# Kernel tuning notes

Hardware: AMD Instinct MI355X
Metric: run time of the kernel (lower is better)

The kernel has to match this reference:

```python
import jax, jax.numpy as jnp
import numpy as np

B = 2
L = 1024
D_MODEL = 1024
D_INNER = 2048   # expand * d_model
D_STATE = 16
DT_RANK = 64     # ceil(d_model / 16)
D_CONV = 4


def setup_inputs() -> dict:
    key = jax.random.key(0)
    ks = jax.random.split(key, 8)
    def nrm(k, shape, scale):
        return jax.random.normal(k, shape, dtype=jnp.float32) * scale
    A_log = jnp.log(jnp.tile(jnp.arange(1, D_STATE + 1, dtype=jnp.float32)[None, :], (D_INNER, 1)))
    return dict(
        hidden_states=jax.random.normal(ks[0], (B, L, D_MODEL), dtype=jnp.float32),
        Win=nrm(ks[1], (D_MODEL, 2 * D_INNER), D_MODEL ** -0.5),
        Wx=nrm(ks[2], (D_INNER, DT_RANK + 2 * D_STATE), D_INNER ** -0.5),
        Wdt=nrm(ks[3], (DT_RANK, D_INNER), DT_RANK ** -0.5),
        dt_bias=nrm(ks[4], (D_INNER,), 1.0),
        Wout=nrm(ks[5], (D_INNER, D_MODEL), D_INNER ** -0.5),
        dw_kernel=nrm(ks[6], (D_CONV, D_INNER), 0.2),
        dw_bias=jnp.zeros((D_INNER,), dtype=jnp.float32),
        A_log=A_log,
        Dskip=jnp.ones((D_INNER,), dtype=jnp.float32),
    )


def _causal_depthwise_conv(x, kernel, bias):
    # x: (B, L, D_INNER), kernel: (k, D_INNER); dilation 1, causal left pad
    k = kernel.shape[0]
    Lq = x.shape[1]
    xpad = jnp.pad(x, ((0, 0), (k - 1, 0), (0, 0)))
    y = sum(xpad[:, i:i + Lq, :] * kernel[i] for i in range(k)) + bias
    return jax.nn.silu(y)


def _selective_scan(u, delta, A, Bm, Cm, Dskip, z):
    # u, delta, z: (B, L, D); A: (D, N); Bm, Cm: (B, L, N)
    deltaA = jnp.exp(jnp.einsum('bld,dn->bldn', delta, A))      # (B,L,D,N)
    deltaBu = jnp.einsum('bld,bln,bld->bldn', delta, Bm, u)     # (B,L,D,N)

    def step(x_prev, elems):
        dA, dBu, c = elems                                      # (B,D,N),(B,D,N),(B,N)
        x_new = dA * x_prev + dBu
        y = jnp.einsum('bdn,bn->bd', x_new, c)
        return x_new, y

    x0 = jnp.zeros((u.shape[0], u.shape[2], A.shape[1]), dtype=jnp.float32)
    _, ys = jax.lax.scan(
        step, x0,
        (deltaA.transpose(1, 0, 2, 3), deltaBu.transpose(1, 0, 2, 3), Cm.transpose(1, 0, 2)))
    y = ys.transpose(1, 0, 2) + u * Dskip                        # skip connection
    return y * jax.nn.silu(z)


def reference(hidden_states, Win, Wx, Wdt, dt_bias, Wout, dw_kernel, dw_bias, A_log, Dskip):
    xz = hidden_states @ Win                                     # (B,L,2*D_INNER)
    x, z = jnp.split(xz, 2, axis=-1)
    A = -jnp.exp(A_log)                                          # (D_INNER, D_STATE)
    x = _causal_depthwise_conv(x, dw_kernel, dw_bias)
    x_dbl = x @ Wx                                               # (B,L,DT_RANK+2*N)
    dt, Bm, Cm = jnp.split(x_dbl, [DT_RANK, DT_RANK + D_STATE], axis=-1)
    delta = jax.nn.softplus(dt @ Wdt + dt_bias)                  # delta_bias + softplus
    y = _selective_scan(x, delta, A, Bm, Cm, Dskip, z)
    return y @ Wout
```

## Files before the change

### kernel.cpp

```cpp
#include <hip/hip_runtime.h>
#include <hip/hip_bf16.h>
#include <math.h>

#define B_SZ 2
#define L_SZ 1024
#define DM 1024
#define DI 2048
#define NS 16
#define DTR 64
#define NCHUNK 16
#define CLEN 64
#define XDLD 128
#define KSPLIT 8

typedef unsigned short ushortT;
typedef __attribute__((ext_vector_type(8))) short short8;
typedef __attribute__((ext_vector_type(4))) float floatx4;

__device__ __forceinline__ ushortT f2bf(float f) {
  unsigned u = __float_as_uint(f);
  unsigned r = (u + 0x7fff + ((u >> 16) & 1)) >> 16;
  return (ushortT)r;
}

__device__ __forceinline__ float bf2f(ushortT v) {
  return __uint_as_float((unsigned)v << 16);
}

__device__ __forceinline__ void gl2lds16(const void* g, void* l) {
  __builtin_amdgcn_global_load_lds(
      (const __attribute__((address_space(1))) unsigned int*)g,
      (__attribute__((address_space(3))) unsigned int*)l, 16, 0, 0);
}

__device__ __forceinline__ unsigned stash_addr(unsigned i) {
  return (i >> 10) * 4096 + 1024 + (i & 1023);
}

__device__ __forceinline__ void tr_body(const float* __restrict__ src,
                                        ushortT* __restrict__ dst, int R, int C,
                                        int bx, int by, int tx, int ty,
                                        float (*t)[33]) {
#pragma unroll
  for (int j = 0; j < 4; ++j)
    t[ty + j * 8][tx] = src[(size_t)(by + ty + j * 8) * C + bx + tx];
  __syncthreads();
#pragma unroll
  for (int j = 0; j < 4; ++j)
    dst[(size_t)(bx + ty + j * 8) * R + by + tx] = f2bf(t[tx][ty + j * 8]);
}

__global__ __launch_bounds__(256) void prep_all(
    const float* __restrict__ hidden, ushortT* __restrict__ hidb,
    const float* __restrict__ Win, ushortT* __restrict__ WinT,
    const float* __restrict__ Wx, ushortT* __restrict__ WxT,
    const float* __restrict__ Wdt, ushortT* __restrict__ WdtT,
    const float* __restrict__ Wout, ushortT* __restrict__ WoutT) {
  __shared__ float t[32][33];
  const int blk = blockIdx.x;
  const int tid = threadIdx.x;
  const int tx = tid & 31, ty = tid >> 5;
  if (blk < 2048) {
    const int i = blk * 256 + tid;
    float4 v = ((const float4*)hidden)[i];
    unsigned lo = (unsigned)f2bf(v.x) | ((unsigned)f2bf(v.y) << 16);
    unsigned hi = (unsigned)f2bf(v.z) | ((unsigned)f2bf(v.w) << 16);
    ((uint2*)hidb)[i] = make_uint2(lo, hi);
  } else if (blk < 6144) {
    const int rel = blk - 2048;
    tr_body(Win, WinT, DM, 2 * DI, (rel & 127) * 32, (rel >> 7) * 32, tx, ty, t);
  } else if (blk < 7168) {
    const int rel = blk - 6144;
    const int k = (rel & 7) * 256 + tid;
    const int n = rel >> 3;
    WxT[(size_t)n * DI + k] = (n < 96) ? f2bf(Wx[(size_t)k * 96 + n]) : (ushortT)0;
  } else if (blk < 7296) {
    const int rel = blk - 7168;
    tr_body(Wdt, WdtT, DTR, DI, (rel & 63) * 32, (rel >> 6) * 32, tx, ty, t);
  } else {
    const int rel = blk - 7296;
    tr_body(Wout, WoutT, DI, DM, (rel & 31) * 32, (rel >> 5) * 32, tx, ty, t);
  }
}

__global__ __launch_bounds__(512) void gemm1_big(
    const ushortT* __restrict__ A, int lda,
    const ushortT* __restrict__ BT, int ldb,
    float* __restrict__ C, int ldc, int K) {
  __shared__ __align__(16) char smem[128 * 128 + 128 * 128];
  char* As = smem;
  char* Bs = smem + 128 * 128;
  const int tid = threadIdx.x;
  const int lane = tid & 63;
  const int quad = lane >> 4;
  const int l16 = lane & 15;
  const int wid = tid >> 6;
  const int wm = wid & 1;
  const int wn = wid >> 1;
  const int m0 = blockIdx.y * 128;
  const int n0 = blockIdx.x * 128;

  floatx4 acc[4][2] = {};

  for (int k0 = 0; k0 < K; k0 += 64) {
    for (int i = tid; i < 128 * 8; i += 512) {
      const int r = i >> 3, c = i & 7;
      const int cg = c ^ (r & 7);
      gl2lds16(A + (size_t)(m0 + r) * lda + k0 + cg * 8, As + (i - lane) * 16);
    }
    for (int i = tid; i < 128 * 8; i += 512) {
      const int r = i >> 3, c = i & 7;
      const int cg = c ^ (r & 7);
      gl2lds16(BT + (size_t)(n0 + r) * ldb + k0 + cg * 8, Bs + (i - lane) * 16);
    }
    __syncthreads();

    short8 afr[4][2], bfr[2][2];
#pragma unroll
    for (int i = 0; i < 4; ++i) {
      const int r = wm * 64 + i * 16 + l16;
#pragma unroll
      for (int s = 0; s < 2; ++s)
        afr[i][s] = *(const short8*)(As + r * 128 + (((s * 4 + quad) ^ (r & 7)) * 16));
    }
#pragma unroll
    for (int j = 0; j < 2; ++j) {
      const int r = wn * 32 + j * 16 + l16;
#pragma unroll
      for (int s = 0; s < 2; ++s)
        bfr[j][s] = *(const short8*)(Bs + r * 128 + (((s * 4 + quad) ^ (r & 7)) * 16));
    }
#pragma unroll
    for (int s = 0; s < 2; ++s)
#pragma unroll
      for (int i = 0; i < 4; ++i)
#pragma unroll
        for (int j = 0; j < 2; ++j)
          acc[i][j] = __builtin_amdgcn_mfma_f32_16x16x32_bf16(afr[i][s], bfr[j][s],
                                                              acc[i][j], 0, 0, 0);
    __syncthreads();
  }
#pragma unroll
  for (int i = 0; i < 4; ++i)
#pragma unroll
    for (int j = 0; j < 2; ++j)
#pragma unroll
      for (int r = 0; r < 4; ++r) {
        const int m = m0 + wm * 64 + i * 16 + quad * 4 + r;
        const int n = n0 + wn * 32 + j * 16 + l16;
        C[(size_t)m * ldc + n] = acc[i][j][r];
      }
}

__global__ __launch_bounds__(256) void gemm_out(
    const ushortT* __restrict__ A, int lda,
    const ushortT* __restrict__ BT, int ldb,
    float* __restrict__ C) {
  __shared__ __align__(16) char smem[64 * 128 + 64 * 128];
  char* As = smem;
  char* Bs = smem + 64 * 128;
  const int tid = threadIdx.x;
  const int lane = tid & 63;
  const int quad = lane >> 4;
  const int l16 = lane & 15;
  const int wid = tid >> 6;
  const int wm = wid & 1;
  const int wn = wid >> 1;
  const int m0 = blockIdx.y * 64;
  const int n0 = blockIdx.x * 64;

  floatx4 acc[2][2] = {};

  for (int k0 = 0; k0 < DI; k0 += 64) {
    for (int i = tid; i < 64 * 8; i += 256) {
      const int r = i >> 3, c = i & 7;
      const int cg = c ^ (r & 7);
      gl2lds16(A + (size_t)(m0 + r) * lda + k0 + cg * 8, As + (i - lane) * 16);
    }
    for (int i = tid; i < 64 * 8; i += 256) {
      const int r = i >> 3, c = i & 7;
      const int cg = c ^ (r & 7);
      gl2lds16(BT + (size_t)(n0 + r) * ldb + k0 + cg * 8, Bs + (i - lane) * 16);
    }
    __syncthreads();

    short8 afr[2][2], bfr[2][2];
#pragma unroll
    for (int i = 0; i < 2; ++i) {
      const int m = wm * 32 + i * 16 + l16;
#pragma unroll
      for (int s = 0; s < 2; ++s)
        afr[i][s] = *(const short8*)(As + m * 128 + (((s * 4 + quad) ^ (m & 7)) * 16));
    }
#pragma unroll
    for (int j = 0; j < 2; ++j) {
      const int n = wn * 32 + j * 16 + l16;
#pragma unroll
      for (int s = 0; s < 2; ++s)
        bfr[j][s] = *(const short8*)(Bs + n * 128 + (((s * 4 + quad) ^ (n & 7)) * 16));
    }
#pragma unroll
    for (int s = 0; s < 2; ++s)
#pragma unroll
      for (int i = 0; i < 2; ++i)
#pragma unroll
        for (int j = 0; j < 2; ++j)
          acc[i][j] = __builtin_amdgcn_mfma_f32_16x16x32_bf16(afr[i][s], bfr[j][s],
                                                              acc[i][j], 0, 0, 0);
    __syncthreads();
  }
#pragma unroll
  for (int i = 0; i < 2; ++i)
#pragma unroll
    for (int j = 0; j < 2; ++j)
#pragma unroll
      for (int r = 0; r < 4; ++r) {
        const int m = m0 + wm * 32 + i * 16 + quad * 4 + r;
        const int n = n0 + wn * 32 + j * 16 + l16;
        C[(size_t)m * DM + n] = acc[i][j][r];
      }
}

__global__ __launch_bounds__(256) void gemm_xdbl_mfma(
    const ushortT* __restrict__ xcb, const ushortT* __restrict__ WxT,
    float* __restrict__ part) {
  __shared__ __align__(16) char smem[64 * 64 + 128 * 64];
  char* As = smem;
  char* Bs = smem + 64 * 64;
  const int tid = threadIdx.x;
  const int lane = tid & 63;
  const int quad = lane >> 4;
  const int l16 = lane & 15;
  const int wid = tid >> 6;
  const int wm = wid & 1;
  const int wn = wid >> 1;
  const int m0 = blockIdx.x * 64;
  const int kbase = blockIdx.y * (DI / KSPLIT);

  floatx4 acc[2][4] = {};

  for (int kk = 0; kk < DI / KSPLIT; kk += 32) {
    const int k0 = kbase + kk;
    for (int i = tid; i < 64 * 4; i += 256) {
      const int r = i >> 2, c = i & 3;
      const int cg = c ^ (r & 3);
      gl2lds16(xcb + (size_t)(m0 + r) * DI + k0 + cg * 8, As + (i - lane) * 16);
    }
    for (int i = tid; i < 128 * 4; i += 256) {
      const int r = i >> 2, c = i & 3;
      const int cg = c ^ (r & 3);
      gl2lds16(WxT + (size_t)r * DI + k0 + cg * 8, Bs + (i - lane) * 16);
    }
    __syncthreads();

    short8 afr[2], bfr[4];
#pragma unroll
    for (int i = 0; i < 2; ++i) {
      const int m = wm * 32 + i * 16 + l16;
      afr[i] = *(const short8*)(As + m * 64 + ((quad ^ (m & 3)) * 16));
    }
#pragma unroll
    for (int j = 0; j < 4; ++j) {
      const int n = wn * 64 + j * 16 + l16;
      bfr[j] = *(const short8*)(Bs + n * 64 + ((quad ^ (n & 3)) * 16));
    }
#pragma unroll
    for (int i = 0; i < 2; ++i)
#pragma unroll
      for (int j = 0; j < 4; ++j)
        acc[i][j] = __builtin_amdgcn_mfma_f32_16x16x32_bf16(afr[i], bfr[j],
                                                            acc[i][j], 0, 0, 0);
    __syncthreads();
  }
  float* out = part + (size_t)blockIdx.y * (B_SZ * L_SZ * XDLD);
#pragma unroll
  for (int i = 0; i < 2; ++i)
#pragma unroll
    for (int j = 0; j < 4; ++j)
#pragma unroll
      for (int r = 0; r < 4; ++r) {
        const int m = m0 + wm * 32 + i * 16 + quad * 4 + r;
        const int n = wn * 64 + j * 16 + l16;
        out[(size_t)m * XDLD + n] = acc[i][j][r];
      }
}

__global__ __launch_bounds__(256) void xdbl_reduce(const float* __restrict__ part,
                                                   float* __restrict__ xdbl,
                                                   ushortT* __restrict__ dtb) {
  const int i = blockIdx.x * 256 + threadIdx.x;
  float4 a = ((const float4*)part)[i];
#pragma unroll
  for (int s = 1; s < KSPLIT; ++s) {
    const float4 b = ((const float4*)part)[(size_t)s * (B_SZ * L_SZ * XDLD / 4) + i];
    a.x += b.x; a.y += b.y; a.z += b.z; a.w += b.w;
  }
  ((float4*)xdbl)[i] = a;
  const int row = i >> 5;
  const int c4 = (i & 31) * 4;
  if (c4 < DTR) {
    const unsigned lo = (unsigned)f2bf(a.x) | ((unsigned)f2bf(a.y) << 16);
    const unsigned hi = (unsigned)f2bf(a.z) | ((unsigned)f2bf(a.w) << 16);
    ((uint2*)dtb)[row * (DTR / 4) + (c4 >> 2)] = make_uint2(lo, hi);
  }
}

__global__ __launch_bounds__(256) void conv_silu(
    const float* __restrict__ xz, const float* __restrict__ kern,
    const float* __restrict__ bias, ushortT* __restrict__ xcb) {
  const int d = blockIdx.y * 256 + threadIdx.x;
  const int b = blockIdx.x >> 7;
  const int l0 = (blockIdx.x & 127) * 8;
  const int row0 = b * L_SZ + l0;
  const float k0v = kern[0 * DI + d], k1v = kern[1 * DI + d];
  const float k2v = kern[2 * DI + d], k3v = kern[3 * DI + d];
  float xv[11];
#pragma unroll
  for (int i = 0; i < 11; ++i) {
    const int l = l0 - 3 + i;
    xv[i] = (l >= 0) ? xz[((size_t)(b * L_SZ + l)) * 4096 + d] : 0.f;
  }
  const float bs = bias[d];
#pragma unroll
  for (int j = 0; j < 8; ++j) {
    float a = bs;
    a = fmaf(xv[j], k0v, a);
    a = fmaf(xv[j + 1], k1v, a);
    a = fmaf(xv[j + 2], k2v, a);
    a = fmaf(xv[j + 3], k3v, a);
    xcb[(size_t)(row0 + j) * DI + d] = f2bf(a / (1.f + __expf(-a)));
  }
}

__global__ __launch_bounds__(256) void gemm_delta_mfma(
    const ushortT* __restrict__ dtb, const ushortT* __restrict__ WdtT,
    const float* __restrict__ dt_bias, float* __restrict__ delta) {
  __shared__ __align__(16) char smem[64 * 128 + 64 * 128];
  char* As = smem;
  char* Bs = smem + 64 * 128;
  const int tid = threadIdx.x;
  const int lane = tid & 63;
  const int quad = lane >> 4;
  const int l16 = lane & 15;
  const int wid = tid >> 6;
  const int wm = wid & 1;
  const int wn = wid >> 1;
  const int m0 = blockIdx.x * 64;
  const int n0 = blockIdx.y * 64;

  for (int i = tid; i < 64 * 8; i += 256) {
    const int r = i >> 3, c = i & 7;
    const int cg = c ^ (r & 7);
    gl2lds16(dtb + (size_t)(m0 + r) * DTR + cg * 8, As + (i - lane) * 16);
  }
  for (int i = tid; i < 64 * 8; i += 256) {
    const int r = i >> 3, c = i & 7;
    const int cg = c ^ (r & 7);
    gl2lds16(WdtT + (size_t)(n0 + r) * DTR + cg * 8, Bs + (i - lane) * 16);
  }
  __syncthreads();

  floatx4 acc[2][2] = {};
  short8 afr[2][2], bfr[2][2];
#pragma unroll
  for (int i = 0; i < 2; ++i) {
    const int m = wm * 32 + i * 16 + l16;
#pragma unroll
    for (int s = 0; s < 2; ++s)
      afr[i][s] = *(const short8*)(As + m * 128 + (((s * 4 + quad) ^ (m & 7)) * 16));
  }
#pragma unroll
  for (int j = 0; j < 2; ++j) {
    const int n = wn * 32 + j * 16 + l16;
#pragma unroll
    for (int s = 0; s < 2; ++s)
      bfr[j][s] = *(const short8*)(Bs + n * 128 + (((s * 4 + quad) ^ (n & 7)) * 16));
  }
#pragma unroll
  for (int s = 0; s < 2; ++s)
#pragma unroll
    for (int i = 0; i < 2; ++i)
#pragma unroll
      for (int j = 0; j < 2; ++j)
        acc[i][j] = __builtin_amdgcn_mfma_f32_16x16x32_bf16(afr[i][s], bfr[j][s],
                                                            acc[i][j], 0, 0, 0);

#pragma unroll
  for (int i = 0; i < 2; ++i)
#pragma unroll
    for (int j = 0; j < 2; ++j) {
      const int n = n0 + wn * 32 + j * 16 + l16;
      const float bias = dt_bias[n];
#pragma unroll
      for (int r = 0; r < 4; ++r) {
        const int m = m0 + wm * 32 + i * 16 + quad * 4 + r;
        const float a = acc[i][j][r] + bias;
        delta[(size_t)m * DI + n] = (a > 20.f) ? a : __logf(1.f + __expf(a));
      }
    }
}

__global__ __launch_bounds__(256) void scan_phase1(
    const float* __restrict__ delta, const ushortT* __restrict__ xcb,
    const float* __restrict__ xdbl, const float* __restrict__ A_log,
    float* __restrict__ xz) {
  const int bx = blockIdx.x;
  const int b = bx >> 9;
  const int c = (bx >> 5) & 15;
  const int dt = bx & 31;
  const int tid = threadIdx.x;
  const int dl = tid >> 2, nq = tid & 3;
  const int d = dt * 64 + dl;
  const int row0 = b * L_SZ + c * CLEN;

  __shared__ float Bsh[CLEN][16];
  for (int i = tid; i < CLEN * 16; i += 256)
    Bsh[i >> 4][i & 15] = xdbl[(size_t)(row0 + (i >> 4)) * XDLD + 64 + (i & 15)];

  float Av[4];
#pragma unroll
  for (int j = 0; j < 4; ++j) Av[j] = -__expf(A_log[d * 16 + nq * 4 + j]);
  float x[4] = {}, P[4] = {1.f, 1.f, 1.f, 1.f};
  __syncthreads();

  const float* dp = delta + (size_t)row0 * DI + d;
  const ushortT* up = xcb + (size_t)row0 * DI + d;
  float dB[4], uB[4];
#pragma unroll
  for (int j = 0; j < 4; ++j) {
    dB[j] = dp[(size_t)j * DI];
    uB[j] = bf2f(up[(size_t)j * DI]);
  }
  for (int l0 = 0; l0 < CLEN; l0 += 4) {
    float dN[4] = {}, uN[4] = {};
    if (l0 + 4 < CLEN) {
#pragma unroll
      for (int j = 0; j < 4; ++j) {
        dN[j] = dp[(size_t)(l0 + 4 + j) * DI];
        uN[j] = bf2f(up[(size_t)(l0 + 4 + j) * DI]);
      }
    }
#pragma unroll
    for (int jj = 0; jj < 4; ++jj) {
      const float dlt = dB[jj];
      const float t = dlt * uB[jj];
      const float* bb = &Bsh[l0 + jj][nq * 4];
#pragma unroll
      for (int n = 0; n < 4; ++n) {
        const float dA = __expf(dlt * Av[n]);
        P[n] *= dA;
        x[n] = fmaf(dA, x[n], t * bb[n]);
      }
    }
#pragma unroll
    for (int j = 0; j < 4; ++j) { dB[j] = dN[j]; uB[j] = uN[j]; }
  }
  const unsigned sb = ((unsigned)((b * NCHUNK + c) * DI + d)) * 16 + nq * 4;
  *(float4*)&xz[stash_addr(sb)] = make_float4(P[0], P[1], P[2], P[3]);
  *(float4*)&xz[stash_addr((1u << 20) + sb)] = make_float4(x[0], x[1], x[2], x[3]);
}

__global__ __launch_bounds__(256) void scan_phase3(
    const float* __restrict__ delta, const ushortT* __restrict__ xcb,
    const float* __restrict__ xdbl, const float* __restrict__ A_log,
    const float* __restrict__ Dskip, float* __restrict__ xz) {
  const int bx = blockIdx.x;
  const int b = bx >> 9;
  const int c = (bx >> 5) & 15;
  const int dt = bx & 31;
  const int tid = threadIdx.x;
  const int dl = tid >> 2, nq = tid & 3;
  const int d = dt * 64 + dl;
  const int row0 = b * L_SZ + c * CLEN;

  __shared__ float Bsh[CLEN][16], Csh[CLEN][16];
  for (int i = tid; i < CLEN * 32; i += 256) {
    const int r = i >> 5, q = i & 31;
    const float v = xdbl[(size_t)(row0 + r) * XDLD + 64 + q];
    if (q < 16) Bsh[r][q] = v; else Csh[r][q - 16] = v;
  }

  float Av[4];
#pragma unroll
  for (int j = 0; j < 4; ++j) Av[j] = -__expf(A_log[d * 16 + nq * 4 + j]);
  const float Dsk = Dskip[d];

  float x[4] = {0.f, 0.f, 0.f, 0.f};
  for (int cc = 0; cc < c; ++cc) {
    const unsigned ib = ((unsigned)((b * NCHUNK + cc) * DI + d)) * 16 + nq * 4;
    const float4 P = *(const float4*)&xz[stash_addr(ib)];
    const float4 S = *(const float4*)&xz[stash_addr((1u << 20) + ib)];
    x[0] = fmaf(P.x, x[0], S.x);
    x[1] = fmaf(P.y, x[1], S.y);
    x[2] = fmaf(P.z, x[2], S.z);
    x[3] = fmaf(P.w, x[3], S.w);
  }
  __syncthreads();

  const float* dp = delta + (size_t)row0 * DI + d;
  const ushortT* up = xcb + (size_t)row0 * DI + d;
  const float* zp = xz + (size_t)row0 * 4096 + DI + d;
  ushortT* yb = (ushortT*)xz;

  float dB[4], uB[4], zB[4];
#pragma unroll
  for (int j = 0; j < 4; ++j) {
    dB[j] = dp[(size_t)j * DI];
    uB[j] = bf2f(up[(size_t)j * DI]);
    zB[j] = zp[(size_t)j * 4096];
  }
  for (int l0 = 0; l0 < CLEN; l0 += 4) {
    float dN[4] = {}, uN[4] = {}, zN[4] = {};
    if (l0 + 4 < CLEN) {
#pragma unroll
      for (int j = 0; j < 4; ++j) {
        dN[j] = dp[(size_t)(l0 + 4 + j) * DI];
        uN[j] = bf2f(up[(size_t)(l0 + 4 + j) * DI]);
        zN[j] = zp[(size_t)(l0 + 4 + j) * 4096];
      }
    }
#pragma unroll
    for (int jj = 0; jj < 4; ++jj) {
      const float dlt = dB[jj];
      const float u = uB[jj];
      const float t = dlt * u;
      const float* bb = &Bsh[l0 + jj][nq * 4];
      const float* cc = &Csh[l0 + jj][nq * 4];
      float y = 0.f;
#pragma unroll
      for (int n = 0; n < 4; ++n) {
        const float dA = __expf(dlt * Av[n]);
        x[n] = fmaf(dA, x[n], t * bb[n]);
        y = fmaf(x[n], cc[n], y);
      }
      y += __shfl_xor(y, 1);
      y += __shfl_xor(y, 2);
      if (nq == 0) {
        const float z = zB[jj];
        const float g = (y + u * Dsk) * (z / (1.f + __expf(-z)));
        yb[(size_t)(row0 + l0 + jj) * 8192 + d] = f2bf(g);
      }
    }
#pragma unroll
    for (int j = 0; j < 4; ++j) { dB[j] = dN[j]; uB[j] = uN[j]; zB[j] = zN[j]; }
  }
}

extern "C" void kernel_launch(void* const* d_in, const int* in_sizes, int n_in,
                              void* d_out, int out_size, void* d_ws, size_t ws_size,
                              hipStream_t stream) {
  const float* hidden  = (const float*)d_in[0];
  const float* Win     = (const float*)d_in[1];
  const float* Wx      = (const float*)d_in[2];
  const float* Wdt     = (const float*)d_in[3];
  const float* dt_bias = (const float*)d_in[4];
  const float* Wout    = (const float*)d_in[5];
  const float* dwk     = (const float*)d_in[6];
  const float* dwb     = (const float*)d_in[7];
  const float* A_log   = (const float*)d_in[8];
  const float* Dskip   = (const float*)d_in[9];

  char* ws = (char*)d_ws;
  float* xz       = (float*)ws;
  float* shared16 = (float*)(ws + (32u << 20));
  ushortT* xcb    = (ushortT*)(ws + (48u << 20));
  ushortT* WoutT  = (ushortT*)(ws + (56u << 20));
  char* dob = (char*)d_out;
  ushortT* hidb = (ushortT*)dob;
  float* xdbl   = (float*)(dob + (4u << 20));
  ushortT* WxT  = (ushortT*)(dob + (5u << 20));
  ushortT* WdtT = (ushortT*)(dob + (5u << 20) + (512u << 10));
  ushortT* dtb  = (ushortT*)(dob + (5u << 20) + (768u << 10));

  prep_all<<<dim3(9344), 256, 0, stream>>>(hidden, hidb, Win, (ushortT*)shared16,
                                           Wx, WxT, Wdt, WdtT, Wout, WoutT);
  gemm1_big<<<dim3(4096 / 128, 2048 / 128), 512, 0, stream>>>(
      hidb, DM, (ushortT*)shared16, DM, xz, 2 * DI, DM);
  conv_silu<<<dim3(B_SZ * L_SZ / 8, DI / 256), 256, 0, stream>>>(xz, dwk, dwb, xcb);
  gemm_xdbl_mfma<<<dim3(B_SZ * L_SZ / 64, KSPLIT), 256, 0, stream>>>(
      xcb, WxT, shared16);
  xdbl_reduce<<<dim3(B_SZ * L_SZ * XDLD / 1024), 256, 0, stream>>>(shared16, xdbl, dtb);
  gemm_delta_mfma<<<dim3(B_SZ * L_SZ / 64, DI / 64), 256, 0, stream>>>(
      dtb, WdtT, dt_bias, shared16);
  scan_phase1<<<dim3(B_SZ * NCHUNK * (DI / 64)), 256, 0, stream>>>(
      shared16, xcb, xdbl, A_log, xz);
  scan_phase3<<<dim3(B_SZ * NCHUNK * (DI / 64)), 256, 0, stream>>>(
      shared16, xcb, xdbl, A_log, Dskip, xz);
  gemm_out<<<dim3(DM / 64, 2048 / 64), 256, 0, stream>>>(
      (ushortT*)xz, 4 * DI, WoutT, DI, (float*)d_out);
}
```

Baseline: 231.7 us.

## Replace two-phase chunked scan with single sequential scan kernel over full sequence

New measurement: 356.8 us. +54.0%, slower.

```diff
diff --git a/kernel.cpp b/kernel.cpp
--- a/kernel.cpp
+++ b/kernel.cpp
@@ -27,14 +27,16 @@
   return __uint_as_float((unsigned)v << 16);
 }
 
+__device__ __forceinline__ float fexp2(float x) {
+  float r;
+  asm("v_exp_f32 %0, %1" : "=v"(r) : "v"(x));
+  return r;
+}
+
 __device__ __forceinline__ void gl2lds16(const void* g, void* l) {
   __builtin_amdgcn_global_load_lds(
       (const __attribute__((address_space(1))) unsigned int*)g,
       (__attribute__((address_space(3))) unsigned int*)l, 16, 0, 0);
-}
-
-__device__ __forceinline__ unsigned stash_addr(unsigned i) {
-  return (i >> 10) * 4096 + 1024 + (i & 1023);
 }
 
 __device__ __forceinline__ void tr_body(const float* __restrict__ src,
@@ -400,149 +402,102 @@
     }
 }
 
-__global__ __launch_bounds__(256) void scan_phase1(
-    const float* __restrict__ delta, const ushortT* __restrict__ xcb,
-    const float* __restrict__ xdbl, const float* __restrict__ A_log,
-    float* __restrict__ xz) {
-  const int bx = blockIdx.x;
-  const int b = bx >> 9;
-  const int c = (bx >> 5) & 15;
-  const int dt = bx & 31;
-  const int tid = threadIdx.x;
-  const int dl = tid >> 2, nq = tid & 3;
-  const int d = dt * 64 + dl;
-  const int row0 = b * L_SZ + c * CLEN;
-
-  __shared__ float Bsh[CLEN][16];
-  for (int i = tid; i < CLEN * 16; i += 256)
-    Bsh[i >> 4][i & 15] = xdbl[(size_t)(row0 + (i >> 4)) * XDLD + 64 + (i & 15)];
-
-  float Av[4];
-#pragma unroll
-  for (int j = 0; j < 4; ++j) Av[j] = -__expf(A_log[d * 16 + nq * 4 + j]);
-  float x[4] = {}, P[4] = {1.f, 1.f, 1.f, 1.f};
-  __syncthreads();
-
-  const float* dp = delta + (size_t)row0 * DI + d;
-  const ushortT* up = xcb + (size_t)row0 * DI + d;
-  float dB[4], uB[4];
-#pragma unroll
-  for (int j = 0; j < 4; ++j) {
-    dB[j] = dp[(size_t)j * DI];
-    uB[j] = bf2f(up[(size_t)j * DI]);
-  }
-  for (int l0 = 0; l0 < CLEN; l0 += 4) {
-    float dN[4] = {}, uN[4] = {};
-    if (l0 + 4 < CLEN) {
-#pragma unroll
-      for (int j = 0; j < 4; ++j) {
-        dN[j] = dp[(size_t)(l0 + 4 + j) * DI];
-        uN[j] = bf2f(up[(size_t)(l0 + 4 + j) * DI]);
-      }
-    }
-#pragma unroll
-    for (int jj = 0; jj < 4; ++jj) {
-      const float dlt = dB[jj];
-      const float t = dlt * uB[jj];
-      const float* bb = &Bsh[l0 + jj][nq * 4];
-#pragma unroll
-      for (int n = 0; n < 4; ++n) {
-        const float dA = __expf(dlt * Av[n]);
-        P[n] *= dA;
-        x[n] = fmaf(dA, x[n], t * bb[n]);
-      }
-    }
-#pragma unroll
-    for (int j = 0; j < 4; ++j) { dB[j] = dN[j]; uB[j] = uN[j]; }
-  }
-  const unsigned sb = ((unsigned)((b * NCHUNK + c) * DI + d)) * 16 + nq * 4;
-  *(float4*)&xz[stash_addr(sb)] = make_float4(P[0], P[1], P[2], P[3]);
-  *(float4*)&xz[stash_addr((1u << 20) + sb)] = make_float4(x[0], x[1], x[2], x[3]);
-}
-
-__global__ __launch_bounds__(256) void scan_phase3(
+__global__ __launch_bounds__(128) void scan_full(
     const float* __restrict__ delta, const ushortT* __restrict__ xcb,
     const float* __restrict__ xdbl, const float* __restrict__ A_log,
     const float* __restrict__ Dskip, float* __restrict__ xz) {
-  const int bx = blockIdx.x;
-  const int b = bx >> 9;
-  const int c = (bx >> 5) & 15;
-  const int dt = bx & 31;
+  __shared__ __align__(16) float BC[2][CLEN][32];
+  const int b = blockIdx.x >> 7;
+  const int d0 = (blockIdx.x & 127) * 16;
   const int tid = threadIdx.x;
-  const int dl = tid >> 2, nq = tid & 3;
-  const int d = dt * 64 + dl;
-  const int row0 = b * L_SZ + c * CLEN;
-
-  __shared__ float Bsh[CLEN][16], Csh[CLEN][16];
-  for (int i = tid; i < CLEN * 32; i += 256) {
-    const int r = i >> 5, q = i & 31;
-    const float v = xdbl[(size_t)(row0 + r) * XDLD + 64 + q];
-    if (q < 16) Bsh[r][q] = v; else Csh[r][q - 16] = v;
-  }
-
-  float Av[4];
-#pragma unroll
-  for (int j = 0; j < 4; ++j) Av[j] = -__expf(A_log[d * 16 + nq * 4 + j]);
+  const int lane = tid & 63;
+  const int nq = tid & 7;
+  const int d = d0 + (tid >> 3);
+  const int rowB = b * L_SZ;
+
+  const float* dp = delta + (size_t)rowB * DI + d;
+  const ushortT* up = xcb + (size_t)rowB * DI + d;
+  const float* zp = xz + (size_t)rowB * 4096 + DI + d;
+  ushortT* yb = (ushortT*)xz;
+
+  float Av2[2];
+#pragma unroll
+  for (int j = 0; j < 2; ++j)
+    Av2[j] = -__expf(A_log[d * 16 + nq * 2 + j]) * 1.44269504f;
   const float Dsk = Dskip[d];
 
-  float x[4] = {0.f, 0.f, 0.f, 0.f};
-  for (int cc = 0; cc < c; ++cc) {
-    const unsigned ib = ((unsigned)((b * NCHUNK + cc) * DI + d)) * 16 + nq * 4;
-    const float4 P = *(const float4*)&xz[stash_addr(ib)];
-    const float4 S = *(const float4*)&xz[stash_addr((1u << 20) + ib)];
-    x[0] = fmaf(P.x, x[0], S.x);
-    x[1] = fmaf(P.y, x[1], S.y);
-    x[2] = fmaf(P.z, x[2], S.z);
-    x[3] = fmaf(P.w, x[3], S.w);
-  }
+  for (int i = tid; i < 512; i += 128) {
+    const int r = i >> 3, q = i & 7;
+    gl2lds16(xdbl + (size_t)(rowB + r) * XDLD + 64 + q * 4,
+             (char*)&BC[0][0][0] + (size_t)(i - lane) * 16);
+  }
+
+  float dB[8];
+  ushortT uB[8];
+#pragma unroll
+  for (int j = 0; j < 8; ++j) {
+    dB[j] = dp[(size_t)j * DI];
+    uB[j] = up[(size_t)j * DI];
+  }
+  float zB = zp[(size_t)nq * 4096];
+  float uzB = bf2f(up[(size_t)nq * DI]);
+
+  float x0 = 0.f, x1 = 0.f;
   __syncthreads();
 
-  const float* dp = delta + (size_t)row0 * DI + d;
-  const ushortT* up = xcb + (size_t)row0 * DI + d;
-  const float* zp = xz + (size_t)row0 * 4096 + DI + d;
-  ushortT* yb = (ushortT*)xz;
-
-  float dB[4], uB[4], zB[4];
-#pragma unroll
-  for (int j = 0; j < 4; ++j) {
-    dB[j] = dp[(size_t)j * DI];
-    uB[j] = bf2f(up[(size_t)j * DI]);
-    zB[j] = zp[(size_t)j * 4096];
-  }
-  for (int l0 = 0; l0 < CLEN; l0 += 4) {
-    float dN[4] = {}, uN[4] = {}, zN[4] = {};
-    if (l0 + 4 < CLEN) {
-#pragma unroll
-      for (int j = 0; j < 4; ++j) {
-        dN[j] = dp[(size_t)(l0 + 4 + j) * DI];
-        uN[j] = bf2f(up[(size_t)(l0 + 4 + j) * DI]);
-        zN[j] = zp[(size_t)(l0 + 4 + j) * 4096];
-      }
-    }
-#pragma unroll
-    for (int jj = 0; jj < 4; ++jj) {
-      const float dlt = dB[jj];
-      const float u = uB[jj];
-      const float t = dlt * u;
-      const float* bb = &Bsh[l0 + jj][nq * 4];
-      const float* cc = &Csh[l0 + jj][nq * 4];
-      float y = 0.f;
-#pragma unroll
-      for (int n = 0; n < 4; ++n) {
-        const float dA = __expf(dlt * Av[n]);
-        x[n] = fmaf(dA, x[n], t * bb[n]);
-        y = fmaf(x[n], cc[n], y);
-      }
-      y += __shfl_xor(y, 1);
-      y += __shfl_xor(y, 2);
-      if (nq == 0) {
-        const float z = zB[jj];
-        const float g = (y + u * Dsk) * (z / (1.f + __expf(-z)));
-        yb[(size_t)(row0 + l0 + jj) * 8192 + d] = f2bf(g);
-      }
-    }
-#pragma unroll
-    for (int j = 0; j < 4; ++j) { dB[j] = dN[j]; uB[j] = uN[j]; zB[j] = zN[j]; }
+  for (int c = 0; c < NCHUNK; ++c) {
+    if (c + 1 < NCHUNK) {
+      const int rb = rowB + (c + 1) * CLEN;
+      for (int i = tid; i < 512; i += 128) {
+        const int r = i >> 3, q = i & 7;
+        gl2lds16(xdbl + (size_t)(rb + r) * XDLD + 64 + q * 4,
+                 (char*)&BC[(c + 1) & 1][0][0] + (size_t)(i - lane) * 16);
+      }
+    }
+    const float(*bc)[32] = BC[c & 1];
+#pragma unroll 1
+    for (int g = 0; g < 8; ++g) {
+      const int gl0 = c * CLEN + g * 8;
+      const int nr = gl0 + 8;
+      float dN[8] = {};
+      ushortT uN[8] = {};
+      float zN = 0.f, uzN = 0.f;
+      if (nr < L_SZ) {
+#pragma unroll
+        for (int j = 0; j < 8; ++j) {
+          dN[j] = dp[(size_t)(nr + j) * DI];
+          uN[j] = up[(size_t)(nr + j) * DI];
+        }
+        zN = zp[(size_t)(nr + nq) * 4096];
+        uzN = bf2f(up[(size_t)(nr + nq) * DI]);
+      }
+      float yk = 0.f;
+#pragma unroll
+      for (int j = 0; j < 8; ++j) {
+        const int l = g * 8 + j;
+        const float2 Bv = *(const float2*)&bc[l][nq * 2];
+        const float2 Cv = *(const float2*)&bc[l][16 + nq * 2];
+        const float dlt = dB[j];
+        const float t = dlt * bf2f(uB[j]);
+        const float dA0 = fexp2(dlt * Av2[0]);
+        const float dA1 = fexp2(dlt * Av2[1]);
+        x0 = fmaf(dA0, x0, t * Bv.x);
+        x1 = fmaf(dA1, x1, t * Bv.y);
+        float y = x0 * Cv.x;
+        y = fmaf(x1, Cv.y, y);
+        y += __shfl_xor(y, 1);
+        y += __shfl_xor(y, 2);
+        y += __shfl_xor(y, 4);
+        yk = (nq == j) ? y : yk;
+      }
+      const float sig = zB / (1.f + __expf(-zB));
+      yb[(size_t)(rowB + gl0 + nq) * 8192 + d] = f2bf(fmaf(uzB, Dsk, yk) * sig);
+#pragma unroll
+      for (int j = 0; j < 8; ++j) { dB[j] = dN[j]; uB[j] = uN[j]; }
+      zB = zN;
+      uzB = uzN;
+    }
+    __syncthreads();
   }
 }
 
@@ -582,10 +537,7 @@
   xdbl_reduce<<<dim3(B_SZ * L_SZ * XDLD / 1024), 256, 0, stream>>>(shared16, xdbl, dtb);
   gemm_delta_mfma<<<dim3(B_SZ * L_SZ / 64, DI / 64), 256, 0, stream>>>(
       dtb, WdtT, dt_bias, shared16);
-  scan_phase1<<<dim3(B_SZ * NCHUNK * (DI / 64)), 256, 0, stream>>>(
-      shared16, xcb, xdbl, A_log, xz);
-  scan_phase3<<<dim3(B_SZ * NCHUNK * (DI / 64)), 256, 0, stream>>>(
-      shared16, xcb, xdbl, A_log, Dskip, xz);
+  scan_full<<<dim3(256), 128, 0, stream>>>(shared16, xcb, xdbl, A_log, Dskip, xz);
   gemm_out<<<dim3(DM / 64, 2048 / 64), 256, 0, stream>>>(
       (ushortT*)xz, 4 * DI, WoutT, DI, (float*)d_out);
 }
```
